# Optimization experiments

Hardware: AMD Instinct MI355X
Metric: run time of the kernel (lower is better)

Reference implementation:

```python
import jax, jax.numpy as jnp
import numpy as np

B, H, D, V = 1024, 4, 128, 100000
EPS = 1e-7  # keras backend epsilon used by SparseCategoricalCrossentropy clipping


def setup_inputs() -> dict:
    key = jax.random.key(0)
    k0, k1, k2, k3, k4 = jax.random.split(key, 5)
    inputs = jax.random.normal(k0, (B, D), dtype=jnp.float32)
    label = jax.random.randint(k1, (B,), 0, V)
    embeddings = jax.random.normal(k2, (V, D), dtype=jnp.float32) * 0.05
    proj_mat = jax.random.normal(k3, (H * D, D), dtype=jnp.float32) * 0.05
    mix_mat = jax.random.normal(k4, (H, D), dtype=jnp.float32) * 0.05
    return {"inputs": inputs, "label": label, "embeddings": embeddings,
            "proj_mat": proj_mat, "mix_mat": mix_mat}


def reference(inputs, label, embeddings, proj_mat, mix_mat):
    # proj: [B, H*D] -> [B, H, D] with tanh nonlinearity
    proj = jnp.tanh(inputs @ proj_mat.T).reshape(-1, H, D)
    # mixture weights pi: [B, H]
    pi = jax.nn.softmax(inputs @ mix_mat.T, axis=-1)
    # per-head full-vocab logits/probs: [B, H, V]
    head_logits = jnp.einsum('bhd,vd->bhv', proj, embeddings)
    head_probs = jax.nn.softmax(head_logits, axis=-1)
    # mixture of softmaxes: [B, V]
    probs = jnp.einsum('bh,bhv->bv', pi, head_probs)
    # sparse categorical cross-entropy on probabilities (not logits)
    p_label = jnp.take_along_axis(probs, label[:, None], axis=1)[:, 0]
    loss = -jnp.mean(jnp.log(jnp.clip(p_label, EPS, 1.0)))
    return probs, loss
```

## Files before the change

### kernel.cpp

```cpp
#include <hip/hip_runtime.h>
#include <hip/hip_bf16.h>
#include <math.h>

#define B_ 1024
#define H_ 4
#define D_ 128
#define V_ 100000
#define M_ (B_*H_)
#define EPS_ 1e-7f

typedef unsigned short ushort_t;
typedef __attribute__((ext_vector_type(4))) float f32x4;
typedef __attribute__((ext_vector_type(8))) short bf16x8;

__device__ __forceinline__ ushort_t f2bf(float f) {
    unsigned u = __float_as_uint(f);
    unsigned r = u + 0x7fffu + ((u >> 16) & 1u);
    return (ushort_t)(r >> 16);
}

__device__ __forceinline__ void gload_lds16(const void* g, void* l) {
    __builtin_amdgcn_global_load_lds(
        (const __attribute__((address_space(1))) unsigned int*)g,
        (__attribute__((address_space(3))) unsigned int*)l,
        16, 0, 0);
}

__global__ __launch_bounds__(512)
void proj_pi_kernel(const float* __restrict__ inputs, const float* __restrict__ proj_mat,
                    const float* __restrict__ mix_mat, ushort_t* __restrict__ Abf,
                    float* __restrict__ pi)
{
    __shared__ float xin[128];
    __shared__ float mixv[4];
    const int b = blockIdx.x, tid = threadIdx.x;
    if (tid < 128) xin[tid] = inputs[b * 128 + tid];
    __syncthreads();

    const float4* row = (const float4*)(proj_mat + tid * 128);
    float acc = 0.f;
#pragma unroll 8
    for (int k = 0; k < 32; ++k) {
        float4 m4 = row[k];
        acc += m4.x * xin[k*4+0] + m4.y * xin[k*4+1] + m4.z * xin[k*4+2] + m4.w * xin[k*4+3];
    }
    Abf[b * 512 + tid] = f2bf(tanhf(acc));

    if (tid < 4) {
        const float4* mrow = (const float4*)(mix_mat + tid * 128);
        float a2 = 0.f;
#pragma unroll 8
        for (int k = 0; k < 32; ++k) {
            float4 m4 = mrow[k];
            a2 += m4.x * xin[k*4+0] + m4.y * xin[k*4+1] + m4.z * xin[k*4+2] + m4.w * xin[k*4+3];
        }
        mixv[tid] = a2;
    }
    __syncthreads();
    if (tid < 4) {
        float m = fmaxf(fmaxf(mixv[0], mixv[1]), fmaxf(mixv[2], mixv[3]));
        float e0 = __expf(mixv[0]-m), e1 = __expf(mixv[1]-m), e2 = __expf(mixv[2]-m), e3 = __expf(mixv[3]-m);
        float s = e0 + e1 + e2 + e3;
        float mye = __expf(mixv[tid]-m);
        pi[b * 4 + tid] = mye / s;
    }
}

__global__ __launch_bounds__(256)
void conv_kernel(const float* __restrict__ e, ushort_t* __restrict__ o, int n4)
{
    int i = blockIdx.x * 256 + threadIdx.x;
    if (i < n4) {
        float4 f = ((const float4*)e)[i];
        ushort4 u;
        u.x = f2bf(f.x); u.y = f2bf(f.y); u.z = f2bf(f.z); u.w = f2bf(f.w);
        ((ushort4*)o)[i] = u;
    }
}

template <int PASS>
__global__ __launch_bounds__(256, 2)
void gemm_kernel(const ushort_t* __restrict__ Abf, const ushort_t* __restrict__ Ebf,
                 const float* __restrict__ pi, float* __restrict__ Z,
                 float* __restrict__ probs)
{
    __shared__ ushort_t lds_a[128 * 128];
    __shared__ ushort_t lds_b[128 * 128];
    __shared__ float w_lds[128];

    const int tid  = threadIdx.x;
    const int wave = tid >> 6;
    const int lane = tid & 63;
    const int q    = lane >> 4;
    const int r16  = lane & 15;
    const int m0   = blockIdx.x * 128;
    const int v0   = blockIdx.y * 128;

    if (PASS == 2) {
        if (tid < 128) {
            int gi = m0 + tid;
            w_lds[tid] = pi[gi] / Z[gi];
        }
    }

#pragma unroll
    for (int t = 0; t < 8; ++t) {
        int r  = t * 16 + (tid >> 4);
        int c  = tid & 15;
        int cs = c ^ (r & 7);
        unsigned loff = (unsigned)__builtin_amdgcn_readfirstlane(t * 4096 + (tid >> 6) * 1024);
        gload_lds16(Abf + (size_t)(m0 + r) * 128 + cs * 8, (char*)lds_a + loff);
        int vrow = v0 + r; if (vrow >= V_) vrow = V_ - 1;
        gload_lds16(Ebf + (size_t)vrow * 128 + cs * 8, (char*)lds_b + loff);
    }
    __syncthreads();

    const int wm = (wave >> 1) * 64;
    const int wn = (wave & 1) * 64;

    f32x4 acc[4][4];
#pragma unroll
    for (int mi = 0; mi < 4; ++mi)
#pragma unroll
        for (int ni = 0; ni < 4; ++ni)
            acc[mi][ni] = (f32x4)(0.f);

#pragma unroll
    for (int kk = 0; kk < 4; ++kk) {
        bf16x8 fa[4], fb[4];
        int chunk = kk * 4 + q;
#pragma unroll
        for (int mi = 0; mi < 4; ++mi) {
            int row = wm + mi * 16 + r16;
            int sc = chunk ^ (row & 7);
            fa[mi] = *(const bf16x8*)&lds_a[row * 128 + sc * 8];
        }
#pragma unroll
        for (int ni = 0; ni < 4; ++ni) {
            int row = wn + ni * 16 + r16;
            int sc = chunk ^ (row & 7);
            fb[ni] = *(const bf16x8*)&lds_b[row * 128 + sc * 8];
        }
#pragma unroll
        for (int mi = 0; mi < 4; ++mi)
#pragma unroll
            for (int ni = 0; ni < 4; ++ni)
                acc[mi][ni] = __builtin_amdgcn_mfma_f32_16x16x32_bf16(fa[mi], fb[ni], acc[mi][ni], 0, 0, 0);
    }

    if (PASS == 1) {
        float zs[4][4];
#pragma unroll
        for (int mi = 0; mi < 4; ++mi)
#pragma unroll
            for (int h = 0; h < 4; ++h) zs[mi][h] = 0.f;

#pragma unroll
        for (int mi = 0; mi < 4; ++mi) {
#pragma unroll
            for (int ni = 0; ni < 4; ++ni) {
                int v = v0 + wn + ni * 16 + r16;
                bool ok = (v < V_);
#pragma unroll
                for (int h = 0; h < 4; ++h) {
                    float e = ok ? __expf(acc[mi][ni][h]) : 0.f;
                    zs[mi][h] += e;
                }
            }
        }
#pragma unroll
        for (int msk = 1; msk < 16; msk <<= 1) {
#pragma unroll
            for (int mi = 0; mi < 4; ++mi)
#pragma unroll
                for (int h = 0; h < 4; ++h)
                    zs[mi][h] += __shfl_xor(zs[mi][h], msk, 64);
        }
        int mi = r16 >> 2, h = r16 & 3;
        int midx = m0 + wm + mi * 16 + q * 4 + h;
        atomicAdd(&Z[midx], zs[mi][h]);
    } else {
#pragma unroll
        for (int mi = 0; mi < 4; ++mi) {
            int mloc = wm + mi * 16 + q * 4;
            float w0 = w_lds[mloc + 0], w1 = w_lds[mloc + 1];
            float w2 = w_lds[mloc + 2], w3 = w_lds[mloc + 3];
            size_t rowoff = (size_t)((m0 + mloc) >> 2) * V_;
#pragma unroll
            for (int ni = 0; ni < 4; ++ni) {
                int v = v0 + wn + ni * 16 + r16;
                if (v < V_) {
                    f32x4 a = acc[mi][ni];
                    float p = w0 * __expf(a[0]) + w1 * __expf(a[1])
                            + w2 * __expf(a[2]) + w3 * __expf(a[3]);
                    probs[rowoff + v] = p;
                }
            }
        }
    }
}

__global__ __launch_bounds__(256)
void loss_kernel(const float* __restrict__ probs, const int* __restrict__ label,
                 float* __restrict__ out)
{
    __shared__ float red[256];
    int tid = threadIdx.x;
    float s = 0.f;
    for (int b = tid; b < B_; b += 256) {
        float p = probs[(size_t)b * V_ + label[b]];
        p = fminf(fmaxf(p, EPS_), 1.0f);
        s -= logf(p);
    }
    red[tid] = s;
    __syncthreads();
    for (int st = 128; st > 0; st >>= 1) {
        if (tid < st) red[tid] += red[tid + st];
        __syncthreads();
    }
    if (tid == 0) out[0] = red[0] / (float)B_;
}

extern "C" void kernel_launch(void* const* d_in, const int* in_sizes, int n_in,
                              void* d_out, int out_size, void* d_ws, size_t ws_size,
                              hipStream_t stream)
{
    const float* inputs   = (const float*)d_in[0];
    const int*   label    = (const int*)d_in[1];
    const float* emb      = (const float*)d_in[2];
    const float* proj_mat = (const float*)d_in[3];
    const float* mix_mat  = (const float*)d_in[4];
    float* out = (float*)d_out;

    char* ws = (char*)d_ws;
    ushort_t* emb_bf = (ushort_t*)ws;
    ushort_t* A_bf   = (ushort_t*)(ws + 25600000);
    float*    pi     = (float*)(ws + 26648576);
    float*    Z      = (float*)(ws + 26664960);

    conv_kernel<<<12500, 256, 0, stream>>>(emb, emb_bf, 3200000);
    proj_pi_kernel<<<1024, 512, 0, stream>>>(inputs, proj_mat, mix_mat, A_bf, pi);
    hipMemsetAsync(Z, 0, 4096 * sizeof(float), stream);

    dim3 g(32, 782);
    gemm_kernel<1><<<g, 256, 0, stream>>>(A_bf, emb_bf, nullptr, Z, nullptr);
    gemm_kernel<2><<<g, 256, 0, stream>>>(A_bf, emb_bf, pi, Z, out);

    loss_kernel<<<1, 256, 0, stream>>>(out, label, out + (size_t)B_ * V_);
}
```

Before: 810.1 us.

## Make GEMM blocks persistent over vocab tiles with double-buffered embedding staging

Each block now keeps its 128-row A tile resident in LDS and iterates over a contiguous range of 64-wide vocab tiles, double-buffering embedding tiles so the next load overlaps current MFMA work. Partition sums stay in registers across tiles, cutting atomics and repeated A/weight loads. log2(e) is folded into the projection so the epilogues use exp2f. Grid shrinks to 512 blocks, which risks low occupancy and less latency hiding for the memory-heavy probs writes.

```diff
diff --git a/kernel.cpp b/kernel.cpp
--- a/kernel.cpp
+++ b/kernel.cpp
@@ -1,5 +1,4 @@
 #include <hip/hip_runtime.h>
-#include <hip/hip_bf16.h>
 #include <math.h>
 
 #define B_ 1024
@@ -8,6 +7,12 @@
 #define V_ 100000
 #define M_ (B_*H_)
 #define EPS_ 1e-7f
+#define LOG2E_ 1.4426950408889634f
+
+#define VT_ 64
+#define NT_ 1563
+#define YB_ 16
+#define TPB_ 98
 
 typedef unsigned short ushort_t;
 typedef __attribute__((ext_vector_type(4))) float f32x4;
@@ -44,7 +49,7 @@
         float4 m4 = row[k];
         acc += m4.x * xin[k*4+0] + m4.y * xin[k*4+1] + m4.z * xin[k*4+2] + m4.w * xin[k*4+3];
     }
-    Abf[b * 512 + tid] = f2bf(tanhf(acc));
+    Abf[b * 512 + tid] = f2bf(LOG2E_ * tanhf(acc));
 
     if (tid < 4) {
         const float4* mrow = (const float4*)(mix_mat + tid * 128);
@@ -78,6 +83,33 @@
     }
 }
 
+__device__ __forceinline__ void stage_a(const ushort_t* __restrict__ Abf, ushort_t* lds_a,
+                                        int m0, int tid, int wave)
+{
+#pragma unroll
+    for (int t = 0; t < 8; ++t) {
+        int r  = t * 16 + (tid >> 4);
+        int c  = tid & 15;
+        int cs = c ^ (r & 7);
+        unsigned loff = (unsigned)__builtin_amdgcn_readfirstlane(t * 4096 + wave * 1024);
+        gload_lds16(Abf + (size_t)(m0 + r) * 128 + cs * 8, (char*)lds_a + loff);
+    }
+}
+
+__device__ __forceinline__ void stage_e(const ushort_t* __restrict__ Ebf, ushort_t* ldsb,
+                                        int v0, int tid, int wave)
+{
+#pragma unroll
+    for (int t = 0; t < 4; ++t) {
+        int r  = t * 16 + (tid >> 4);
+        int c  = tid & 15;
+        int cs = c ^ (r & 7);
+        int vrow = v0 + r; if (vrow >= V_) vrow = V_ - 1;
+        unsigned loff = (unsigned)__builtin_amdgcn_readfirstlane(t * 4096 + wave * 1024);
+        gload_lds16(Ebf + (size_t)vrow * 128 + cs * 8, (char*)ldsb + loff);
+    }
+}
+
 template <int PASS>
 __global__ __launch_bounds__(256, 2)
 void gemm_kernel(const ushort_t* __restrict__ Abf, const ushort_t* __restrict__ Ebf,
@@ -85,7 +117,7 @@
                  float* __restrict__ probs)
 {
     __shared__ ushort_t lds_a[128 * 128];
-    __shared__ ushort_t lds_b[128 * 128];
+    __shared__ ushort_t lds_e[2][64 * 128];
     __shared__ float w_lds[128];
 
     const int tid  = threadIdx.x;
@@ -94,80 +126,108 @@
     const int q    = lane >> 4;
     const int r16  = lane & 15;
     const int m0   = blockIdx.x * 128;
-    const int v0   = blockIdx.y * 128;
-
+    const int wm   = (wave >> 1) * 64;
+    const int wn   = (wave & 1) * 32;
+
+    const int t_begin = blockIdx.y * TPB_;
+    int t_end = t_begin + TPB_; if (t_end > NT_) t_end = NT_;
+
+    if (PASS == 2 && tid < 128) {
+        int gi = m0 + tid;
+        w_lds[tid] = pi[gi] / Z[gi];
+    }
+
+    stage_a(Abf, lds_a, m0, tid, wave);
+    stage_e(Ebf, lds_e[0], t_begin * VT_, tid, wave);
+    __syncthreads();
+
+    float wreg[4][4];
     if (PASS == 2) {
-        if (tid < 128) {
-            int gi = m0 + tid;
-            w_lds[tid] = pi[gi] / Z[gi];
-        }
-    }
-
-#pragma unroll
-    for (int t = 0; t < 8; ++t) {
-        int r  = t * 16 + (tid >> 4);
-        int c  = tid & 15;
-        int cs = c ^ (r & 7);
-        unsigned loff = (unsigned)__builtin_amdgcn_readfirstlane(t * 4096 + (tid >> 6) * 1024);
-        gload_lds16(Abf + (size_t)(m0 + r) * 128 + cs * 8, (char*)lds_a + loff);
-        int vrow = v0 + r; if (vrow >= V_) vrow = V_ - 1;
-        gload_lds16(Ebf + (size_t)vrow * 128 + cs * 8, (char*)lds_b + loff);
-    }
-    __syncthreads();
-
-    const int wm = (wave >> 1) * 64;
-    const int wn = (wave & 1) * 64;
-
-    f32x4 acc[4][4];
-#pragma unroll
-    for (int mi = 0; mi < 4; ++mi)
-#pragma unroll
-        for (int ni = 0; ni < 4; ++ni)
-            acc[mi][ni] = (f32x4)(0.f);
-
-#pragma unroll
-    for (int kk = 0; kk < 4; ++kk) {
-        bf16x8 fa[4], fb[4];
-        int chunk = kk * 4 + q;
-#pragma unroll
-        for (int mi = 0; mi < 4; ++mi) {
-            int row = wm + mi * 16 + r16;
-            int sc = chunk ^ (row & 7);
-            fa[mi] = *(const bf16x8*)&lds_a[row * 128 + sc * 8];
-        }
-#pragma unroll
-        for (int ni = 0; ni < 4; ++ni) {
-            int row = wn + ni * 16 + r16;
-            int sc = chunk ^ (row & 7);
-            fb[ni] = *(const bf16x8*)&lds_b[row * 128 + sc * 8];
-        }
 #pragma unroll
         for (int mi = 0; mi < 4; ++mi)
 #pragma unroll
-            for (int ni = 0; ni < 4; ++ni)
-                acc[mi][ni] = __builtin_amdgcn_mfma_f32_16x16x32_bf16(fa[mi], fb[ni], acc[mi][ni], 0, 0, 0);
-    }
-
+            for (int j = 0; j < 4; ++j)
+                wreg[mi][j] = w_lds[wm + mi * 16 + q * 4 + j];
+    }
+
+    float zs[4][4];
     if (PASS == 1) {
-        float zs[4][4];
 #pragma unroll
         for (int mi = 0; mi < 4; ++mi)
 #pragma unroll
             for (int h = 0; h < 4; ++h) zs[mi][h] = 0.f;
-
-#pragma unroll
-        for (int mi = 0; mi < 4; ++mi) {
-#pragma unroll
-            for (int ni = 0; ni < 4; ++ni) {
-                int v = v0 + wn + ni * 16 + r16;
-                bool ok = (v < V_);
-#pragma unroll
-                for (int h = 0; h < 4; ++h) {
-                    float e = ok ? __expf(acc[mi][ni][h]) : 0.f;
-                    zs[mi][h] += e;
+    }
+
+    int bb = 0;
+    for (int vt = t_begin; vt < t_end; ++vt) {
+        if (vt + 1 < t_end)
+            stage_e(Ebf, lds_e[bb ^ 1], (vt + 1) * VT_, tid, wave);
+
+        f32x4 acc[4][2];
+#pragma unroll
+        for (int mi = 0; mi < 4; ++mi)
+#pragma unroll
+            for (int ni = 0; ni < 2; ++ni) acc[mi][ni] = (f32x4)(0.f);
+
+#pragma unroll
+        for (int kk = 0; kk < 4; ++kk) {
+            int chunk = kk * 4 + q;
+            bf16x8 fa[4], fb[2];
+#pragma unroll
+            for (int mi = 0; mi < 4; ++mi) {
+                int row = wm + mi * 16 + r16;
+                int sc  = chunk ^ (row & 7);
+                fa[mi] = *(const bf16x8*)&lds_a[row * 128 + sc * 8];
+            }
+#pragma unroll
+            for (int ni = 0; ni < 2; ++ni) {
+                int row = wn + ni * 16 + r16;
+                int sc  = chunk ^ (row & 7);
+                fb[ni] = *(const bf16x8*)&lds_e[bb][row * 128 + sc * 8];
+            }
+#pragma unroll
+            for (int mi = 0; mi < 4; ++mi)
+#pragma unroll
+                for (int ni = 0; ni < 2; ++ni)
+                    acc[mi][ni] = __builtin_amdgcn_mfma_f32_16x16x32_bf16(fa[mi], fb[ni], acc[mi][ni], 0, 0, 0);
+        }
+
+        __syncthreads();
+
+        if (PASS == 1) {
+#pragma unroll
+            for (int mi = 0; mi < 4; ++mi)
+#pragma unroll
+                for (int ni = 0; ni < 2; ++ni) {
+                    int v = vt * VT_ + wn + ni * 16 + r16;
+                    bool ok = (v < V_);
+#pragma unroll
+                    for (int h = 0; h < 4; ++h) {
+                        float e = exp2f(acc[mi][ni][h]);
+                        zs[mi][h] += ok ? e : 0.f;
+                    }
+                }
+        } else {
+#pragma unroll
+            for (int mi = 0; mi < 4; ++mi) {
+                int mloc = wm + mi * 16 + q * 4;
+                size_t rowoff = (size_t)((m0 + mloc) >> 2) * V_;
+#pragma unroll
+                for (int ni = 0; ni < 2; ++ni) {
+                    int v = vt * VT_ + wn + ni * 16 + r16;
+                    if (v < V_) {
+                        f32x4 a = acc[mi][ni];
+                        float p = wreg[mi][0] * exp2f(a[0]) + wreg[mi][1] * exp2f(a[1])
+                                + wreg[mi][2] * exp2f(a[2]) + wreg[mi][3] * exp2f(a[3]);
+                        probs[rowoff + v] = p;
+                    }
                 }
             }
         }
+        bb ^= 1;
+    }
+
+    if (PASS == 1) {
 #pragma unroll
         for (int msk = 1; msk < 16; msk <<= 1) {
 #pragma unroll
@@ -179,24 +239,6 @@
         int mi = r16 >> 2, h = r16 & 3;
         int midx = m0 + wm + mi * 16 + q * 4 + h;
         atomicAdd(&Z[midx], zs[mi][h]);
-    } else {
-#pragma unroll
-        for (int mi = 0; mi < 4; ++mi) {
-            int mloc = wm + mi * 16 + q * 4;
-            float w0 = w_lds[mloc + 0], w1 = w_lds[mloc + 1];
-            float w2 = w_lds[mloc + 2], w3 = w_lds[mloc + 3];
-            size_t rowoff = (size_t)((m0 + mloc) >> 2) * V_;
-#pragma unroll
-            for (int ni = 0; ni < 4; ++ni) {
-                int v = v0 + wn + ni * 16 + r16;
-                if (v < V_) {
-                    f32x4 a = acc[mi][ni];
-                    float p = w0 * __expf(a[0]) + w1 * __expf(a[1])
-                            + w2 * __expf(a[2]) + w3 * __expf(a[3]);
-                    probs[rowoff + v] = p;
-                }
-            }
-        }
     }
 }
 
@@ -242,7 +284,7 @@
     proj_pi_kernel<<<1024, 512, 0, stream>>>(inputs, proj_mat, mix_mat, A_bf, pi);
     hipMemsetAsync(Z, 0, 4096 * sizeof(float), stream);
 
-    dim3 g(32, 782);
+    dim3 g(32, YB_);
     gemm_kernel<1><<<g, 256, 0, stream>>>(A_bf, emb_bf, nullptr, Z, nullptr);
     gemm_kernel<2><<<g, 256, 0, stream>>>(A_bf, emb_bf, pi, Z, out);
 
```

Measured after the change: 840.8 us. +3.8%, slower.
